# Optimization experiments

Hardware: AMD Instinct MI355X
Metric: run time of the kernel (lower is better)

Reference implementation:

```python
import jax, jax.numpy as jnp
import numpy as np

B, S, HID = 2, 4096, 1024
NH, HD = 16, 64
R = 2  # dilation_rate


def setup_inputs() -> dict:
    key = jax.random.key(0)
    ks = jax.random.split(key, 6)
    sc = 0.02
    return {
        "hidden_states": jax.random.normal(ks[0], (B, S, HID), jnp.float32),
        "Wq": jax.random.normal(ks[1], (HID, HID), jnp.float32) * sc,
        "Wk": jax.random.normal(ks[2], (HID, HID), jnp.float32) * sc,
        "Wv": jax.random.normal(ks[3], (HID, HID), jnp.float32) * sc,
        "Wo": jax.random.normal(ks[4], (HID, HID), jnp.float32) * sc,
        "bo": jnp.zeros((HID,), jnp.float32),
    }


def reference(hidden_states, Wq, Wk, Wv, Wo, bo):
    bsz, q_len, _ = hidden_states.shape
    # projections (torch Linear: y = x @ W.T)
    q = jnp.einsum('bsh,oh->bso', hidden_states, Wq).reshape(bsz, q_len, NH, HD).transpose(0, 2, 1, 3)
    k = jnp.einsum('bsh,oh->bso', hidden_states, Wk).reshape(bsz, q_len, NH, HD).transpose(0, 2, 1, 3)
    v = jnp.einsum('bsh,oh->bso', hidden_states, Wv).reshape(bsz, q_len, NH, HD).transpose(0, 2, 1, 3)
    # strided dilation gather (indices 0, R, 2R, ...)
    q = q[:, :, ::R, :]
    k = k[:, :, ::R, :]
    v = v[:, :, ::R, :]
    sd = q.shape[2]  # dilated length
    # SDPA with is_causal=True over the dilated subsequence
    scores = jnp.einsum('bhqd,bhkd->bhqk', q, k) / np.sqrt(HD).astype(np.float32)
    causal = jnp.tril(jnp.ones((sd, sd), bool))
    scores = jnp.where(causal, scores, jnp.finfo(scores.dtype).min)
    probs = jax.nn.softmax(scores, axis=-1)
    attn = jnp.einsum('bhqk,bhkd->bhqd', probs, v)  # [B, H, sd, HD]
    attn = attn.transpose(0, 2, 1, 3).reshape(bsz, sd, HID)
    # scatter back into zero-initialized full-length tensor
    full = jnp.zeros((bsz, q_len, HID), attn.dtype).at[:, ::R, :].set(attn)
    return jnp.einsum('bsh,oh->bso', full, Wo) + bo
```

## Files before the change

kernel.cpp:

```cpp
#include <hip/hip_runtime.h>
#include <cstdint>

typedef unsigned short u16;
typedef unsigned int u32;
typedef __attribute__((ext_vector_type(8))) short short8;
typedef __attribute__((ext_vector_type(4))) float f32x4;
typedef __attribute__((ext_vector_type(4))) unsigned short u16x4;

#define S_ 4096
#define SD 2048

__device__ __forceinline__ u16 f2bf(float f) {
  union { float f; u32 u; } v; v.f = f;
  u32 r = v.u + 0x7fffu + ((v.u >> 16) & 1u);
  return (u16)(r >> 16);
}
__device__ __forceinline__ u32 pk2bf(float a, float b) {
  union { float f; u32 u; } ua, ub; ua.f = a; ub.f = b;
  return __builtin_amdgcn_perm(ub.u + 0x8000u, ua.u + 0x8000u, 0x07060302u);
}
__device__ __forceinline__ f32x4 mfma16(short8 a, short8 b, f32x4 c) {
  return __builtin_amdgcn_mfma_f32_16x16x32_bf16(a, b, c, 0, 0, 0);
}
__device__ __forceinline__ void async16(const void* g, void* l) {
  __builtin_amdgcn_global_load_lds((__attribute__((address_space(1))) void*)g,
                                   (__attribute__((address_space(3))) void*)l,
                                   16, 0, 0);
}

__global__ __launch_bounds__(256) void cast_all(const float* __restrict__ hs,
                                                const float* __restrict__ Wq,
                                                const float* __restrict__ Wk,
                                                const float* __restrict__ Wv,
                                                const float* __restrict__ Wo,
                                                u16* __restrict__ dstW,
                                                u16* __restrict__ dstX) {
  int bid = blockIdx.x;
  if (bid < 4096) {
    int gid = bid * 256 + threadIdx.x;
    int wsel = gid >> 18;
    int off  = (gid & 262143) * 4;
    const float* src = (wsel == 0) ? Wq : (wsel == 1) ? Wk : (wsel == 2) ? Wv : Wo;
    float scl = (wsel == 0) ? 0.18033688f : 1.0f;
    f32x4 v = *(const f32x4*)(src + off);
    u16x4 o; o.x = f2bf(v.x * scl); o.y = f2bf(v.y * scl);
    o.z = f2bf(v.z * scl); o.w = f2bf(v.w * scl);
    *(u16x4*)(dstW + (size_t)wsel * 1048576 + off) = o;
  } else {
    int gid = (bid - 4096) * 256 + threadIdx.x;
    int e = gid * 4;
    int m = e >> 10, col = e & 1023;
    int b = m >> 11, sm = m & 2047;
    const float* src = hs + ((size_t)(b * S_ + 2 * sm) << 10) + col;
    f32x4 v = *(const f32x4*)src;
    u16x4 o; o.x = f2bf(v.x); o.y = f2bf(v.y); o.z = f2bf(v.z); o.w = f2bf(v.w);
    *(u16x4*)(dstX + ((size_t)m << 10) + col) = o;
  }
}

__device__ __forceinline__ void gemm_body128(const u16* __restrict__ A,
                                             const u16* __restrict__ B,
                                             u16* __restrict__ C, int N,
                                             int bm, int bn, char* lA, char* lB) {
  const int tid = threadIdx.x, lane = tid & 63, w = tid >> 6;
  const int quad = lane >> 4, l15 = lane & 15;
  const int wm = (w & 1) * 64, wn = (w >> 1) * 64;
  f32x4 acc[4][4] = {};

  auto stage = [&](int buf, int k0) {
#pragma unroll
    for (int i = 0; i < 2; i++) {
      int p = i * 256 + tid;
      int row = p >> 2, cp = p & 3;
      int c = cp ^ ((row ^ (row >> 2)) & 3);
      async16(A + (size_t)(bm + row) * 1024 + k0 + c * 8,
              lA + buf * 8192 + i * 4096 + w * 1024);
      async16(B + (size_t)(bn + row) * 1024 + k0 + c * 8,
              lB + buf * 8192 + i * 4096 + w * 1024);
    }
  };

  stage(0, 0);
#pragma unroll 1
  for (int kt = 0; kt < 32; kt++) {
    __syncthreads();
    if (kt + 1 < 32) stage((kt + 1) & 1, (kt + 1) * 32);
    const char* A_ = lA + (kt & 1) * 8192;
    const char* B_ = lB + (kt & 1) * 8192;
    short8 af[4], bf[4];
#pragma unroll
    for (int mi = 0; mi < 4; mi++) {
      int row = wm + mi * 16 + l15;
      af[mi] = *(const short8*)(A_ + (row * 4 + (quad ^ ((row ^ (row >> 2)) & 3))) * 16);
    }
#pragma unroll
    for (int ni = 0; ni < 4; ni++) {
      int row = wn + ni * 16 + l15;
      bf[ni] = *(const short8*)(B_ + (row * 4 + (quad ^ ((row ^ (row >> 2)) & 3))) * 16);
    }
#pragma unroll
    for (int mi = 0; mi < 4; mi++)
#pragma unroll
      for (int ni = 0; ni < 4; ni++)
        acc[mi][ni] = mfma16(af[mi], bf[ni], acc[mi][ni]);
  }
#pragma unroll
  for (int mi = 0; mi < 4; mi++)
#pragma unroll
    for (int ni = 0; ni < 4; ni++) {
      int m0 = bm + wm + mi * 16 + quad * 4;
      int n = bn + wn + ni * 16 + l15;
#pragma unroll
      for (int r = 0; r < 4; r++)
        C[(size_t)(m0 + r) * N + n] = f2bf(acc[mi][ni][r]);
    }
}

__global__ __launch_bounds__(256) void qkv_gemm(const u16* __restrict__ X,
                                                const u16* __restrict__ Wbf,
                                                u16* __restrict__ QK,
                                                u16* __restrict__ Vt) {
  __shared__ __align__(16) char lA[16384];
  __shared__ __align__(16) char lB[16384];
  int bid = blockIdx.x;
  if (bid < 512) {
    gemm_body128(X, Wbf, QK, 2048, (bid >> 4) * 128, (bid & 15) * 128, lA, lB);
  } else {
    int b2 = bid - 512;
    gemm_body128(Wbf + 2 * 1048576, X, Vt, 4096, (b2 >> 5) * 128, (b2 & 31) * 128, lA, lB);
  }
}

__global__ __launch_bounds__(256) void oproj(const u16* __restrict__ A,
                                             const u16* __restrict__ B,
                                             const float* __restrict__ bo,
                                             float* __restrict__ out) {
  __shared__ __align__(16) char lA[2 * 4096];
  __shared__ __align__(16) char lB[2 * 8192];
  const int tid = threadIdx.x, lane = tid & 63, w = tid >> 6;
  const int quad = lane >> 4, l15 = lane & 15;
  const int bm = blockIdx.y * 64, bn = blockIdx.x * 128;
  const int wm = (w & 1) * 32, wn = (w >> 1) * 64;
  f32x4 acc[2][4] = {};

  auto stage = [&](int buf, int k0) {
    {
      int p = tid;
      int row = p >> 2, cp = p & 3;
      int c = cp ^ ((row ^ (row >> 2)) & 3);
      async16(A + (size_t)(bm + row) * 1024 + k0 + c * 8, lA + buf * 4096 + w * 1024);
    }
#pragma unroll
    for (int i = 0; i < 2; i++) {
      int p = i * 256 + tid;
      int row = p >> 2, cp = p & 3;
      int c = cp ^ ((row ^ (row >> 2)) & 3);
      async16(B + (size_t)(bn + row) * 1024 + k0 + c * 8, lB + buf * 8192 + i * 4096 + w * 1024);
    }
  };

  stage(0, 0);
#pragma unroll 1
  for (int kt = 0; kt < 32; kt++) {
    __syncthreads();
    if (kt + 1 < 32) stage((kt + 1) & 1, (kt + 1) * 32);
    const char* A_ = lA + (kt & 1) * 4096;
    const char* B_ = lB + (kt & 1) * 8192;
    short8 af[2], bf[4];
#pragma unroll
    for (int mi = 0; mi < 2; mi++) {
      int row = wm + mi * 16 + l15;
      af[mi] = *(const short8*)(A_ + (row * 4 + (quad ^ ((row ^ (row >> 2)) & 3))) * 16);
    }
#pragma unroll
    for (int ni = 0; ni < 4; ni++) {
      int row = wn + ni * 16 + l15;
      bf[ni] = *(const short8*)(B_ + (row * 4 + (quad ^ ((row ^ (row >> 2)) & 3))) * 16);
    }
#pragma unroll
    for (int mi = 0; mi < 2; mi++)
#pragma unroll
      for (int ni = 0; ni < 4; ni++)
        acc[mi][ni] = mfma16(af[mi], bf[ni], acc[mi][ni]);
  }
#pragma unroll
  for (int mi = 0; mi < 2; mi++)
#pragma unroll
    for (int ni = 0; ni < 4; ni++) {
      int n = bn + wn + ni * 16 + l15;
      float bias = bo[n];
#pragma unroll
      for (int r = 0; r < 4; r++) {
        int m = bm + wm + mi * 16 + quad * 4 + r;
        int bb = m >> 11, sm = m & 2047;
        size_t grow = ((size_t)(bb * S_ + 2 * sm)) << 10;
        out[grow + n] = acc[mi][ni][r] + bias;
        out[grow + 1024 + n] = bias;
      }
    }
}

__global__ __launch_bounds__(256) void attn3(const u16* __restrict__ QK,
                                             const u16* __restrict__ Vt,
                                             u16* __restrict__ O) {
  __shared__ __align__(16) char lK[2][8192];
  __shared__ __align__(16) char lV[2][8192];
  __shared__ __align__(16) char lP[4][2048];
  const int tid = threadIdx.x, lane = tid & 63, w = tid >> 6;
  const int quad = lane >> 4, l15 = lane & 15;
  const int h = blockIdx.x, b = blockIdx.y;
  const int qt = 31 - (int)blockIdx.z;
  const int qb = qt * 64 + w * 16;
  const int sw = l15 & 7;

  const u16* qp = QK + (size_t)(b * SD + qb + l15) * 2048 + h * 64 + quad * 8;
  short8 qf0 = *(const short8*)qp;
  short8 qf1 = *(const short8*)(qp + 32);

  auto stage = [&](int buf, int kb) {
#pragma unroll
    for (int i = 0; i < 2; i++) {
      int p = (w * 2 + i) * 64 + lane;
      int row = p >> 3, c = (p & 7) ^ (row & 7);
      async16(QK + (size_t)(b * SD + kb + row) * 2048 + 1024 + h * 64 + c * 8,
              lK[buf] + (w * 2 + i) * 1024);
      async16(Vt + (size_t)(h * 64 + row) * 4096 + b * SD + kb + c * 8,
              lV[buf] + (w * 2 + i) * 1024);
    }
  };

  f32x4 oacc[4] = {};
  float l4[4] = {0.f, 0.f, 0.f, 0.f};
  char* Pw = lP[w];

  stage(0, 0);
#pragma unroll 1
  for (int kt = 0; kt <= qt; kt++) {
    __syncthreads();
    if (kt + 1 <= qt) stage((kt + 1) & 1, (kt + 1) * 64);
    const char* K_ = lK[kt & 1];
    const char* V_ = lV[kt & 1];

    f32x4 s[4];
#pragma unroll
    for (int m = 0; m < 4; m++) {
      int key = m * 16 + l15;
      short8 kf0 = *(const short8*)(K_ + (key * 8 + (quad ^ (key & 7))) * 16);
      short8 kf1 = *(const short8*)(K_ + (key * 8 + ((4 + quad) ^ (key & 7))) * 16);
      f32x4 a = {};
      a = mfma16(kf0, qf0, a);
      a = mfma16(kf1, qf1, a);
      s[m] = a;
    }
    if (kt == qt) {
      int qrel = w * 16 + l15;
#pragma unroll
      for (int m = 0; m < 4; m++)
#pragma unroll
        for (int r = 0; r < 4; r++)
          if (m * 16 + quad * 4 + r > qrel) s[m][r] = -1e30f;
    }
    float pr[4][4];
#pragma unroll
    for (int m = 0; m < 4; m++) {
#pragma unroll
      for (int r = 0; r < 4; r++) pr[m][r] = exp2f(s[m][r]);
      l4[m] += (pr[m][0] + pr[m][1]) + (pr[m][2] + pr[m][3]);
    }
#pragma unroll
    for (int m = 0; m < 4; m++) {
      int c = m * 2 + (quad >> 1);
      int base = l15 * 128 + ((c ^ sw) * 16) + (quad & 1) * 8;
      *(u32*)(Pw + base)     = pk2bf(pr[m][0], pr[m][1]);
      *(u32*)(Pw + base + 4) = pk2bf(pr[m][2], pr[m][3]);
    }
    short8 pf0 = *(const short8*)(Pw + l15 * 128 + ((quad ^ sw) * 16));
    short8 pf1 = *(const short8*)(Pw + l15 * 128 + (((4 + quad) ^ sw) * 16));

#pragma unroll
    for (int m = 0; m < 4; m++) {
      int dim = m * 16 + l15;
      short8 vf0 = *(const short8*)(V_ + (dim * 8 + (quad ^ (dim & 7))) * 16);
      short8 vf1 = *(const short8*)(V_ + (dim * 8 + ((4 + quad) ^ (dim & 7))) * 16);
      oacc[m] = mfma16(vf0, pf0, oacc[m]);
      oacc[m] = mfma16(vf1, pf1, oacc[m]);
    }
  }
  float l = (l4[0] + l4[1]) + (l4[2] + l4[3]);
  l += __shfl_xor(l, 16, 64);
  l += __shfl_xor(l, 32, 64);
  float inv = 1.0f / l;
  u16* op = O + (size_t)(b * SD + qb + l15) * 1024 + h * 64;
#pragma unroll
  for (int m = 0; m < 4; m++) {
    u16x4 ov;
#pragma unroll
    for (int r = 0; r < 4; r++) ov[r] = f2bf(oacc[m][r] * inv);
    *(u16x4*)(op + m * 16 + quad * 4) = ov;
  }
}

extern "C" void kernel_launch(void* const* d_in, const int* in_sizes, int n_in,
                              void* d_out, int out_size, void* d_ws, size_t ws_size,
                              hipStream_t stream) {
  (void)in_sizes; (void)n_in; (void)out_size; (void)ws_size;
  const float* hs = (const float*)d_in[0];
  const float* Wq = (const float*)d_in[1];
  const float* Wk = (const float*)d_in[2];
  const float* Wv = (const float*)d_in[3];
  const float* Wo = (const float*)d_in[4];
  const float* bo = (const float*)d_in[5];
  float* out = (float*)d_out;
  char* ws = (char*)d_ws;

  u16* Xbf = (u16*)ws;
  u16* Wbf = (u16*)(ws + (8u << 20));
  u16* QKb = (u16*)(ws + (16u << 20));
  u16* Vtb = (u16*)(ws + (32u << 20));
  u16* Ob  = (u16*)(ws + (40u << 20));

  cast_all<<<8192, 256, 0, stream>>>(hs, Wq, Wk, Wv, Wo, Wbf, Xbf);
  qkv_gemm<<<768, 256, 0, stream>>>(Xbf, Wbf, QKb, Vtb);
  attn3<<<dim3(16, 2, 32), 256, 0, stream>>>(QKb, Vtb, Ob);
  oproj<<<dim3(8, 64), 256, 0, stream>>>(Ob, Wbf + 3 * 1048576, bo, out);
}
```

Measured before the change: 192.1 us.

## Keep P in registers via permuted V staging and shrink oproj tile

The attention kernel stops round-tripping the probability tile through LDS. V is now loaded through registers and written to LDS in a permuted key order, so the packed bf16 P values from the QK^T MFMA output can feed the PV MFMA directly as the B operand. P packing uses the hardware cvt_pk_bf16_f32 builtin when the compiler provides it. The output projection tile drops from 64x128 to 64x64, doubling the grid for better CU occupancy at the cost of more A-tile reloads; the V path also gives up async global-to-LDS copies and adds register pressure.

```diff
diff --git a/kernel.cpp b/kernel.cpp
--- a/kernel.cpp
+++ b/kernel.cpp
@@ -6,6 +6,8 @@
 typedef __attribute__((ext_vector_type(8))) short short8;
 typedef __attribute__((ext_vector_type(4))) float f32x4;
 typedef __attribute__((ext_vector_type(4))) unsigned short u16x4;
+typedef __attribute__((ext_vector_type(4))) u32 u32x4;
+typedef __attribute__((ext_vector_type(2))) u32 u32x2;
 
 #define S_ 4096
 #define SD 2048
@@ -15,10 +17,17 @@
   u32 r = v.u + 0x7fffu + ((v.u >> 16) & 1u);
   return (u16)(r >> 16);
 }
-__device__ __forceinline__ u32 pk2bf(float a, float b) {
+#if __has_builtin(__builtin_amdgcn_cvt_pk_bf16_f32)
+__device__ __forceinline__ u32 pkbf(float a, float b) {
+  auto r = __builtin_amdgcn_cvt_pk_bf16_f32(a, b);
+  u32 o; __builtin_memcpy(&o, &r, 4); return o;
+}
+#else
+__device__ __forceinline__ u32 pkbf(float a, float b) {
   union { float f; u32 u; } ua, ub; ua.f = a; ub.f = b;
   return __builtin_amdgcn_perm(ub.u + 0x8000u, ua.u + 0x8000u, 0x07060302u);
 }
+#endif
 __device__ __forceinline__ f32x4 mfma16(short8 a, short8 b, f32x4 c) {
   return __builtin_amdgcn_mfma_f32_16x16x32_bf16(a, b, c, 0, 0, 0);
 }
@@ -135,28 +144,19 @@
                                              const u16* __restrict__ B,
                                              const float* __restrict__ bo,
                                              float* __restrict__ out) {
-  __shared__ __align__(16) char lA[2 * 4096];
-  __shared__ __align__(16) char lB[2 * 8192];
+  __shared__ __align__(16) char lA[8192];
+  __shared__ __align__(16) char lB[8192];
   const int tid = threadIdx.x, lane = tid & 63, w = tid >> 6;
   const int quad = lane >> 4, l15 = lane & 15;
-  const int bm = blockIdx.y * 64, bn = blockIdx.x * 128;
-  const int wm = (w & 1) * 32, wn = (w >> 1) * 64;
-  f32x4 acc[2][4] = {};
+  const int bm = blockIdx.y * 64, bn = blockIdx.x * 64;
+  const int wm = (w & 1) * 32, wn = (w >> 1) * 32;
+  f32x4 acc[2][2] = {};
 
   auto stage = [&](int buf, int k0) {
-    {
-      int p = tid;
-      int row = p >> 2, cp = p & 3;
-      int c = cp ^ ((row ^ (row >> 2)) & 3);
-      async16(A + (size_t)(bm + row) * 1024 + k0 + c * 8, lA + buf * 4096 + w * 1024);
-    }
-#pragma unroll
-    for (int i = 0; i < 2; i++) {
-      int p = i * 256 + tid;
-      int row = p >> 2, cp = p & 3;
-      int c = cp ^ ((row ^ (row >> 2)) & 3);
-      async16(B + (size_t)(bn + row) * 1024 + k0 + c * 8, lB + buf * 8192 + i * 4096 + w * 1024);
-    }
+    int row = tid >> 2, cp = tid & 3;
+    int c = cp ^ ((row ^ (row >> 2)) & 3);
+    async16(A + (size_t)(bm + row) * 1024 + k0 + c * 8, lA + buf * 4096 + w * 1024);
+    async16(B + (size_t)(bn + row) * 1024 + k0 + c * 8, lB + buf * 4096 + w * 1024);
   };
 
   stage(0, 0);
@@ -165,28 +165,28 @@
     __syncthreads();
     if (kt + 1 < 32) stage((kt + 1) & 1, (kt + 1) * 32);
     const char* A_ = lA + (kt & 1) * 4096;
-    const char* B_ = lB + (kt & 1) * 8192;
-    short8 af[2], bf[4];
+    const char* B_ = lB + (kt & 1) * 4096;
+    short8 af[2], bf[2];
 #pragma unroll
     for (int mi = 0; mi < 2; mi++) {
       int row = wm + mi * 16 + l15;
       af[mi] = *(const short8*)(A_ + (row * 4 + (quad ^ ((row ^ (row >> 2)) & 3))) * 16);
     }
 #pragma unroll
-    for (int ni = 0; ni < 4; ni++) {
+    for (int ni = 0; ni < 2; ni++) {
       int row = wn + ni * 16 + l15;
       bf[ni] = *(const short8*)(B_ + (row * 4 + (quad ^ ((row ^ (row >> 2)) & 3))) * 16);
     }
 #pragma unroll
     for (int mi = 0; mi < 2; mi++)
 #pragma unroll
-      for (int ni = 0; ni < 4; ni++)
+      for (int ni = 0; ni < 2; ni++)
         acc[mi][ni] = mfma16(af[mi], bf[ni], acc[mi][ni]);
   }
 #pragma unroll
   for (int mi = 0; mi < 2; mi++)
 #pragma unroll
-    for (int ni = 0; ni < 4; ni++) {
+    for (int ni = 0; ni < 2; ni++) {
       int n = bn + wn + ni * 16 + l15;
       float bias = bo[n];
 #pragma unroll
@@ -200,44 +200,69 @@
     }
 }
 
-__global__ __launch_bounds__(256) void attn3(const u16* __restrict__ QK,
+__global__ __launch_bounds__(256) void attn6(const u16* __restrict__ QK,
                                              const u16* __restrict__ Vt,
                                              u16* __restrict__ O) {
   __shared__ __align__(16) char lK[2][8192];
   __shared__ __align__(16) char lV[2][8192];
-  __shared__ __align__(16) char lP[4][2048];
   const int tid = threadIdx.x, lane = tid & 63, w = tid >> 6;
   const int quad = lane >> 4, l15 = lane & 15;
   const int h = blockIdx.x, b = blockIdx.y;
   const int qt = 31 - (int)blockIdx.z;
   const int qb = qt * 64 + w * 16;
-  const int sw = l15 & 7;
 
   const u16* qp = QK + (size_t)(b * SD + qb + l15) * 2048 + h * 64 + quad * 8;
   short8 qf0 = *(const short8*)qp;
   short8 qf1 = *(const short8*)(qp + 32);
 
-  auto stage = [&](int buf, int kb) {
+  auto stageK = [&](int buf, int kb) {
 #pragma unroll
     for (int i = 0; i < 2; i++) {
       int p = (w * 2 + i) * 64 + lane;
       int row = p >> 3, c = (p & 7) ^ (row & 7);
       async16(QK + (size_t)(b * SD + kb + row) * 2048 + 1024 + h * 64 + c * 8,
               lK[buf] + (w * 2 + i) * 1024);
-      async16(Vt + (size_t)(h * 64 + row) * 4096 + b * SD + kb + c * 8,
-              lV[buf] + (w * 2 + i) * 1024);
-    }
+    }
+  };
+
+  const int vd = tid >> 2, vg = tid & 3;
+  const u16* vgbase = Vt + (size_t)(h * 64 + vd) * 4096 + b * SD;
+  const int vs = vd & 7;
+  const int cb0 = (vg & 1) * 2;
+  const int cb1 = cb0 + 4;
+  const int inn = (vg >> 1) * 8;
+  const int aw0 = vd * 128 + ((cb0     ^ vs) * 16) + inn;
+  const int aw1 = vd * 128 + (((cb0+1) ^ vs) * 16) + inn;
+  const int aw2 = vd * 128 + ((cb1     ^ vs) * 16) + inn;
+  const int aw3 = vd * 128 + (((cb1+1) ^ vs) * 16) + inn;
+
+  u32x4 nv0, nv1;
+  auto loadV = [&](int kb) {
+    nv0 = *(const u32x4*)(vgbase + kb + vg * 8);
+    nv1 = *(const u32x4*)(vgbase + kb + 32 + vg * 8);
+  };
+  auto writeV = [&](int buf) {
+    char* Vn = lV[buf];
+    *(u32x2*)(Vn + aw0) = u32x2{nv0.x, nv0.y};
+    *(u32x2*)(Vn + aw1) = u32x2{nv0.z, nv0.w};
+    *(u32x2*)(Vn + aw2) = u32x2{nv1.x, nv1.y};
+    *(u32x2*)(Vn + aw3) = u32x2{nv1.z, nv1.w};
   };
 
   f32x4 oacc[4] = {};
   float l4[4] = {0.f, 0.f, 0.f, 0.f};
-  char* Pw = lP[w];
-
-  stage(0, 0);
+
+  stageK(0, 0);
+  loadV(0);
+  writeV(0);
+
 #pragma unroll 1
   for (int kt = 0; kt <= qt; kt++) {
     __syncthreads();
-    if (kt + 1 <= qt) stage((kt + 1) & 1, (kt + 1) * 64);
+    if (kt + 1 <= qt) {
+      stageK((kt + 1) & 1, (kt + 1) * 64);
+      loadV((kt + 1) * 64);
+    }
     const char* K_ = lK[kt & 1];
     const char* V_ = lV[kt & 1];
 
@@ -267,25 +292,27 @@
       for (int r = 0; r < 4; r++) pr[m][r] = exp2f(s[m][r]);
       l4[m] += (pr[m][0] + pr[m][1]) + (pr[m][2] + pr[m][3]);
     }
+    u32 pw[8];
 #pragma unroll
     for (int m = 0; m < 4; m++) {
-      int c = m * 2 + (quad >> 1);
-      int base = l15 * 128 + ((c ^ sw) * 16) + (quad & 1) * 8;
-      *(u32*)(Pw + base)     = pk2bf(pr[m][0], pr[m][1]);
-      *(u32*)(Pw + base + 4) = pk2bf(pr[m][2], pr[m][3]);
-    }
-    short8 pf0 = *(const short8*)(Pw + l15 * 128 + ((quad ^ sw) * 16));
-    short8 pf1 = *(const short8*)(Pw + l15 * 128 + (((4 + quad) ^ sw) * 16));
+      pw[m * 2]     = pkbf(pr[m][0], pr[m][1]);
+      pw[m * 2 + 1] = pkbf(pr[m][2], pr[m][3]);
+    }
+    short8 pf0, pf1;
+    __builtin_memcpy(&pf0, &pw[0], 16);
+    __builtin_memcpy(&pf1, &pw[4], 16);
 
 #pragma unroll
     for (int m = 0; m < 4; m++) {
-      int dim = m * 16 + l15;
-      short8 vf0 = *(const short8*)(V_ + (dim * 8 + (quad ^ (dim & 7))) * 16);
-      short8 vf1 = *(const short8*)(V_ + (dim * 8 + ((4 + quad) ^ (dim & 7))) * 16);
+      int dr = m * 16 + l15;
+      short8 vf0 = *(const short8*)(V_ + (dr * 128 + ((quad     ^ (dr & 7)) * 16)));
+      short8 vf1 = *(const short8*)(V_ + (dr * 128 + (((4+quad) ^ (dr & 7)) * 16)));
       oacc[m] = mfma16(vf0, pf0, oacc[m]);
       oacc[m] = mfma16(vf1, pf1, oacc[m]);
     }
-  }
+    if (kt + 1 <= qt) writeV((kt + 1) & 1);
+  }
+
   float l = (l4[0] + l4[1]) + (l4[2] + l4[3]);
   l += __shfl_xor(l, 16, 64);
   l += __shfl_xor(l, 32, 64);
@@ -321,6 +348,6 @@
 
   cast_all<<<8192, 256, 0, stream>>>(hs, Wq, Wk, Wv, Wo, Wbf, Xbf);
   qkv_gemm<<<768, 256, 0, stream>>>(Xbf, Wbf, QKb, Vtb);
-  attn3<<<dim3(16, 2, 32), 256, 0, stream>>>(QKb, Vtb, Ob);
-  oproj<<<dim3(8, 64), 256, 0, stream>>>(Ob, Wbf + 3 * 1048576, bo, out);
-}
+  attn6<<<dim3(16, 2, 32), 256, 0, stream>>>(QKb, Vtb, Ob);
+  oproj<<<dim3(16, 64), 256, 0, stream>>>(Ob, Wbf + 3 * 1048576, bo, out);
+}
```

Result: no change. 190.6 us (-0.8%).
